# Optimization experiments

Measured on AMD Instinct MI355X. Metric: run time of the kernel, lower is better.

## Reference

```python
import jax, jax.numpy as jnp
import numpy as np

N = 1024
D = 128          # node_dim
NUM_LAYERS = 3
H_CLS = 128      # edge classifier hidden


def setup_inputs() -> dict:
    key = jax.random.key(0)
    ks = jax.random.split(key, 20)
    s_in = 1.0 / np.sqrt(3.0)
    s_d = 1.0 / np.sqrt(D)
    s_2d = 1.0 / np.sqrt(2 * D)
    s_h = 1.0 / np.sqrt(H_CLS)
    inp = {
        "node_features": jax.random.uniform(ks[0], (N, 3), jnp.float32),
        "adj_matrix": jax.random.uniform(ks[1], (N, N), jnp.float32),
        "edge_weights": jax.random.normal(ks[2], (N, N, 1), jnp.float32),
        # node embedding Linear(3, D)
        "W_embed": jax.random.uniform(ks[3], (3, D), jnp.float32, -s_in, s_in),
        "b_embed": jax.random.uniform(ks[4], (D,), jnp.float32, -s_in, s_in),
        # stacked GCN layer params, [L, ...]
        "Wu": jax.random.uniform(ks[5], (NUM_LAYERS, D, D), jnp.float32, -s_d, s_d),
        "bu": jax.random.uniform(ks[6], (NUM_LAYERS, D), jnp.float32, -s_d, s_d),
        "Wv": jax.random.uniform(ks[7], (NUM_LAYERS, D, D), jnp.float32, -s_d, s_d),
        "bv": jax.random.uniform(ks[8], (NUM_LAYERS, D), jnp.float32, -s_d, s_d),
        "Wg": jax.random.uniform(ks[9], (NUM_LAYERS, 2 * D, D), jnp.float32, -s_2d, s_2d),
        "bg": jax.random.uniform(ks[10], (NUM_LAYERS, D), jnp.float32, -s_2d, s_2d),
        # edge classifier: Linear(2D, 128) -> ReLU -> Linear(128, 1)
        "Wc1": jax.random.uniform(ks[11], (2 * D, H_CLS), jnp.float32, -s_2d, s_2d),
        "bc1": jax.random.uniform(ks[12], (H_CLS,), jnp.float32, -s_2d, s_2d),
        "Wc2": jax.random.uniform(ks[13], (H_CLS, 1), jnp.float32, -s_h, s_h),
        "bc2": jax.random.uniform(ks[14], (1,), jnp.float32, -s_h, s_h),
    }
    return inp


def reference(node_features, adj_matrix, edge_weights,
              W_embed, b_embed, Wu, bu, Wv, bv, Wg, bg,
              Wc1, bc1, Wc2, bc2):
    h = node_features @ W_embed + b_embed                       # [N, D]
    for l in range(NUM_LAYERS):
        u = h @ Wu[l] + bu[l]                                   # [N, D]
        v = h @ Wv[l] + bv[l]                                   # [N, D]
        agg = adj_matrix @ v                                    # [N, D]
        # gate Linear(2D, D) on cat([u, agg]) == u @ Wg[:D] + agg @ Wg[D:]
        gate = jax.nn.sigmoid(u @ Wg[l, :D] + agg @ Wg[l, D:] + bg[l])
        h = jax.nn.relu(h + gate * agg)
    # edge classifier: cat([h_i, h_j]) @ Wc1 == (h @ Wc1[:D])[i] + (h @ Wc1[D:])[j]
    hi = h @ Wc1[:D]                                            # [N, H]
    hj = h @ Wc1[D:]                                            # [N, H]
    hidden = jax.nn.relu(hi[:, None, :] + hj[None, :, :] + bc1) # [N, N, H]
    logits = jnp.einsum('ijh,h->ij', hidden, Wc2[:, 0]) + bc2[0]  # [N, N]
    loss = jnp.mean(jnp.square(logits * adj_matrix - edge_weights[..., 0]))
    return logits, loss
```

## Files before the change

kernel.cpp:

```cpp
#include <hip/hip_runtime.h>

#define NN 1024
#define DD 128

typedef __attribute__((ext_vector_type(8))) __bf16 bf16x8;
typedef __attribute__((ext_vector_type(4))) float f32x4;

__device__ __forceinline__ float us2f(unsigned short b) { return __uint_as_float(((unsigned)b) << 16); }
__device__ __forceinline__ unsigned short f2bf(float f) {
    unsigned x = __float_as_uint(f);
    unsigned r = (x + 0x7fffu + ((x >> 16) & 1u)) >> 16;
    return (unsigned short)r;
}

__global__ __launch_bounds__(256) void k_prep(
    const float* __restrict__ adj, unsigned short* __restrict__ aH, unsigned short* __restrict__ aL)
{
    int idx = (blockIdx.x * 256 + threadIdx.x) * 4;
    float4 a = *(const float4*)(adj + idx);
    ushort4 hv, lv;
    hv.x = f2bf(a.x); lv.x = f2bf(a.x - us2f(hv.x));
    hv.y = f2bf(a.y); lv.y = f2bf(a.y - us2f(hv.y));
    hv.z = f2bf(a.z); lv.z = f2bf(a.z - us2f(hv.z));
    hv.w = f2bf(a.w); lv.w = f2bf(a.w - us2f(hv.w));
    *(ushort4*)(aH + idx) = hv;
    *(ushort4*)(aL + idx) = lv;
}

__global__ __launch_bounds__(256) void k_embed(
    const float* __restrict__ nf, const float* __restrict__ We,
    const float* __restrict__ be, float* __restrict__ h)
{
    int tid = threadIdx.x;
    int m = blockIdx.x * 2 + (tid >> 7);
    int d = tid & 127;
    float a = be[d];
#pragma unroll
    for (int k = 0; k < 3; ++k) a = fmaf(nf[m * 3 + k], We[k * DD + d], a);
    h[m * DD + d] = a;
}

__global__ __launch_bounds__(256) void k_uv(
    const float* __restrict__ h,
    const float* __restrict__ Wu, const float* __restrict__ bu,
    const float* __restrict__ Wv, const float* __restrict__ bv,
    float* __restrict__ u, unsigned short* __restrict__ vTh, unsigned short* __restrict__ vTl)
{
    int tid = threadIdx.x;
    int d = tid & 127, half = tid >> 7;
    int m0 = blockIdx.x * 4;
    const float* W = half ? Wv : Wu;
    const float* A = h + m0 * DD;
    float acc[4] = {0.f, 0.f, 0.f, 0.f};
#pragma unroll 8
    for (int k = 0; k < DD; ++k) {
        float w = W[k * DD + d];
#pragma unroll
        for (int r = 0; r < 4; ++r) acc[r] = fmaf(A[r * DD + k], w, acc[r]);
    }
    if (half == 0) {
        float bb = bu[d];
#pragma unroll
        for (int r = 0; r < 4; ++r) u[(m0 + r) * DD + d] = acc[r] + bb;
    } else {
        float bb = bv[d];
        ushort4 hv, lv;
        float v0 = acc[0] + bb, v1 = acc[1] + bb, v2 = acc[2] + bb, v3 = acc[3] + bb;
        hv.x = f2bf(v0); lv.x = f2bf(v0 - us2f(hv.x));
        hv.y = f2bf(v1); lv.y = f2bf(v1 - us2f(hv.y));
        hv.z = f2bf(v2); lv.z = f2bf(v2 - us2f(hv.z));
        hv.w = f2bf(v3); lv.w = f2bf(v3 - us2f(hv.w));
        *(ushort4*)(vTh + d * NN + m0) = hv;
        *(ushort4*)(vTl + d * NN + m0) = lv;
    }
}

__global__ __launch_bounds__(64) void k_agg(
    const unsigned short* __restrict__ adjH, const unsigned short* __restrict__ adjL,
    const unsigned short* __restrict__ vTh, const unsigned short* __restrict__ vTl,
    float* __restrict__ agg)
{
    int lane = threadIdx.x;
    int b = blockIdx.x;
    int nt = (b >> 3) & 7;
    int mt = (b & 7) | ((b >> 6) << 3);
    int m = lane & 15, quad = lane >> 4;
    const unsigned short* ah = adjH + (size_t)(mt * 16 + m) * NN + quad * 8;
    const unsigned short* al = adjL + (size_t)(mt * 16 + m) * NN + quad * 8;
    const unsigned short* bh = vTh + (size_t)(nt * 16 + m) * NN + quad * 8;
    const unsigned short* bl = vTl + (size_t)(nt * 16 + m) * NN + quad * 8;
    f32x4 acc = {0.f, 0.f, 0.f, 0.f};
#pragma unroll 4
    for (int kt = 0; kt < 32; ++kt) {
        bf16x8 aH = *(const bf16x8*)(ah + kt * 32);
        bf16x8 aL = *(const bf16x8*)(al + kt * 32);
        bf16x8 bH = *(const bf16x8*)(bh + kt * 32);
        bf16x8 bL = *(const bf16x8*)(bl + kt * 32);
        acc = __builtin_amdgcn_mfma_f32_16x16x32_bf16(aH, bH, acc, 0, 0, 0);
        acc = __builtin_amdgcn_mfma_f32_16x16x32_bf16(aH, bL, acc, 0, 0, 0);
        acc = __builtin_amdgcn_mfma_f32_16x16x32_bf16(aL, bH, acc, 0, 0, 0);
    }
    int row0 = mt * 16 + quad * 4;
    int col = nt * 16 + m;
#pragma unroll
    for (int r = 0; r < 4; ++r) agg[(row0 + r) * DD + col] = acc[r];
}

__global__ __launch_bounds__(256) void k_gate(
    const float* __restrict__ u, const float* __restrict__ agg,
    const float* __restrict__ Wg, const float* __restrict__ bg,
    float* __restrict__ h)
{
    int tid = threadIdx.x;
    int d = tid & 127, rh = tid >> 7;
    int m0 = blockIdx.x * 4 + rh * 2;
    const float* WA = Wg;
    const float* WB = Wg + DD * DD;
    const float* Au = u + m0 * DD;
    const float* Ag = agg + m0 * DD;
    float acc[2] = {0.f, 0.f};
#pragma unroll 8
    for (int k = 0; k < DD; ++k) {
        float wa = WA[k * DD + d];
        float wb = WB[k * DD + d];
#pragma unroll
        for (int r = 0; r < 2; ++r)
            acc[r] = fmaf(Au[r * DD + k], wa, fmaf(Ag[r * DD + k], wb, acc[r]));
    }
    float bgd = bg[d];
#pragma unroll
    for (int r = 0; r < 2; ++r) {
        float z = acc[r] + bgd;
        float g = 1.f / (1.f + __expf(-z));
        float av = agg[(m0 + r) * DD + d];
        float hv = h[(m0 + r) * DD + d];
        float nh = fmaf(g, av, hv);
        h[(m0 + r) * DD + d] = nh > 0.f ? nh : 0.f;
    }
}

__global__ __launch_bounds__(256) void k_cls(
    const float* __restrict__ h,
    const float* __restrict__ Wc1, const float* __restrict__ bc1,
    const float* __restrict__ Wc2,
    float* __restrict__ hi, float* __restrict__ hj,
    float* __restrict__ S1, float* __restrict__ S2)
{
    __shared__ float sred[2][4];
    int tid = threadIdx.x;
    int hh = tid & 127, half = tid >> 7;
    int m0 = blockIdx.x * 4;
    if (tid < 8) sred[tid >> 2][tid & 3] = 0.f;
    __syncthreads();
    const float* W = Wc1 + (half ? DD * DD : 0);
    const float* A = h + m0 * DD;
    float acc[4] = {0.f, 0.f, 0.f, 0.f};
#pragma unroll 8
    for (int k = 0; k < DD; ++k) {
        float w = W[k * DD + hh];
#pragma unroll
        for (int r = 0; r < 4; ++r) acc[r] = fmaf(A[r * DD + k], w, acc[r]);
    }
    float wv = Wc2[hh];
    float bcv = half ? 0.f : bc1[hh];
    float* out = half ? hj : hi;
#pragma unroll
    for (int r = 0; r < 4; ++r) {
        float val = acc[r] + bcv;
        out[(m0 + r) * DD + hh] = val;
        float p = val * wv;
#pragma unroll
        for (int off = 32; off; off >>= 1) p += __shfl_down(p, off);
        if ((tid & 63) == 0) atomicAdd(&sred[half][r], p);
    }
    __syncthreads();
    if (tid < 4) S1[m0 + tid] = sred[0][tid];
    else if (tid < 8) S2[m0 + tid - 4] = sred[1][tid - 4];
}

__global__ __launch_bounds__(256) void k_edge(
    const float* __restrict__ hi, const float* __restrict__ hj,
    const float* __restrict__ S1, const float* __restrict__ S2,
    const float* __restrict__ Wc2, const float* __restrict__ bc2,
    const float* __restrict__ adj, const float* __restrict__ ew,
    float* __restrict__ outL, float* __restrict__ lossAcc)
{
    __shared__ float hiT[128][68];
    __shared__ float hjT[128][68];
    __shared__ float wS[128];
    __shared__ float lred;
    int tid = threadIdx.x;
    int i0 = (blockIdx.x >> 4) * 64, j0 = (blockIdx.x & 15) * 64;
    if (tid == 0) lred = 0.f;
    if (tid < 128) wS[tid] = Wc2[tid];
    for (int e = tid; e < 64 * 128; e += 256) {
        int r = e >> 7, hh = e & 127;
        hiT[hh][r] = hi[(i0 + r) * DD + hh];
        hjT[hh][r] = hj[(j0 + r) * DD + hh];
    }
    __syncthreads();
    int tx = tid & 15, ty = tid >> 4;
    float acc[4][4] = {};
#pragma unroll 4
    for (int hh = 0; hh < 128; ++hh) {
        f32x4 a = *(const f32x4*)&hiT[hh][ty * 4];
        f32x4 b = *(const f32x4*)&hjT[hh][tx * 4];
        float w = wS[hh];
#pragma unroll
        for (int p = 0; p < 4; ++p)
#pragma unroll
            for (int q = 0; q < 4; ++q) {
                float x = a[p] + b[q];
                acc[p][q] = fmaf(fabsf(x), w, acc[p][q]);
            }
    }
    float bcv = bc2[0];
    float ls = 0.f;
#pragma unroll
    for (int p = 0; p < 4; ++p) {
        int i = i0 + ty * 4 + p;
        float s1 = S1[i];
        int jb = j0 + tx * 4;
        f32x4 s2 = *(const f32x4*)(S2 + jb);
        f32x4 lg;
#pragma unroll
        for (int q = 0; q < 4; ++q)
            lg[q] = fmaf(0.5f, acc[p][q] + s1 + s2[q], bcv);
        *(f32x4*)(outL + (size_t)i * NN + jb) = lg;
        f32x4 a4 = *(const f32x4*)(adj + (size_t)i * NN + jb);
        f32x4 e4 = *(const f32x4*)(ew + (size_t)i * NN + jb);
#pragma unroll
        for (int q = 0; q < 4; ++q) {
            float t = fmaf(lg[q], a4[q], -e4[q]);
            ls = fmaf(t, t, ls);
        }
    }
#pragma unroll
    for (int off = 32; off; off >>= 1) ls += __shfl_down(ls, off);
    if ((tid & 63) == 0) atomicAdd(&lred, ls);
    __syncthreads();
    if (tid == 0) atomicAdd(lossAcc, lred);
}

__global__ void k_loss(const float* __restrict__ lossAcc, float* __restrict__ outL)
{
    if (threadIdx.x == 0 && blockIdx.x == 0)
        outL[(size_t)NN * NN] = lossAcc[0] * (1.f / (1024.f * 1024.f));
}

extern "C" void kernel_launch(void* const* d_in, const int* in_sizes, int n_in,
                              void* d_out, int out_size, void* d_ws, size_t ws_size,
                              hipStream_t stream)
{
    const float* nf  = (const float*)d_in[0];
    const float* adj = (const float*)d_in[1];
    const float* ew  = (const float*)d_in[2];
    const float* We  = (const float*)d_in[3];
    const float* be  = (const float*)d_in[4];
    const float* Wu  = (const float*)d_in[5];
    const float* bu  = (const float*)d_in[6];
    const float* Wv  = (const float*)d_in[7];
    const float* bv  = (const float*)d_in[8];
    const float* Wg  = (const float*)d_in[9];
    const float* bg  = (const float*)d_in[10];
    const float* Wc1 = (const float*)d_in[11];
    const float* bc1 = (const float*)d_in[12];
    const float* Wc2 = (const float*)d_in[13];
    const float* bc2 = (const float*)d_in[14];

    float* ws = (float*)d_ws;
    float* h   = ws;
    float* u   = ws + 131072;
    unsigned short* vTh = (unsigned short*)(ws + 262144);
    unsigned short* vTl = (unsigned short*)(ws + 327680);
    float* agg = ws + 393216;
    unsigned short* adjH = (unsigned short*)(ws + 524288);
    unsigned short* adjL = (unsigned short*)(ws + 1048576);
    float* S1  = ws + 1572864;
    float* S2  = ws + 1573888;
    float* lossAcc = ws + 1574912;
    float* hi = u;
    float* hj = agg;

    hipMemsetAsync(lossAcc, 0, sizeof(float), stream);
    k_prep<<<1024, 256, 0, stream>>>(adj, adjH, adjL);
    k_embed<<<512, 256, 0, stream>>>(nf, We, be, h);
    for (int l = 0; l < 3; ++l) {
        k_uv<<<256, 256, 0, stream>>>(h, Wu + l * 16384, bu + l * 128,
                                      Wv + l * 16384, bv + l * 128, u, vTh, vTl);
        k_agg<<<512, 64, 0, stream>>>(adjH, adjL, vTh, vTl, agg);
        k_gate<<<256, 256, 0, stream>>>(u, agg, Wg + l * 32768, bg + l * 128, h);
    }
    k_cls<<<256, 256, 0, stream>>>(h, Wc1, bc1, Wc2, hi, hj, S1, S2);
    k_edge<<<256, 256, 0, stream>>>(hi, hj, S1, S2, Wc2, bc2, adj, ew,
                                    (float*)d_out, lossAcc);
    k_loss<<<1, 64, 0, stream>>>(lossAcc, (float*)d_out);
}
```

Baseline: 208.2 us.

## Fuse per-layer kernels, split-K the aggregation, fold loss finalize into edge kernel

Merges the adjacency split, embedding and first u/v projection into one launch. The gate of layer l is fused with the u/v projection of layer l+1, and the last gate with the classifier projection. The adjacency aggregation becomes an 8-way split-K over 1024 blocks writing partial sums that the gate kernel reduces. The memset and the separate loss kernel are replaced by a last-block counter inside the edge kernel. This removes many launches and adds parallelism to the skinny aggregation GEMM, at the cost of extra partial-sum traffic (8x N×D floats) and a redundant per-block embedding recompute.

```diff
diff --git a/kernel.cpp b/kernel.cpp
--- a/kernel.cpp
+++ b/kernel.cpp
@@ -9,54 +9,64 @@
 __device__ __forceinline__ float us2f(unsigned short b) { return __uint_as_float(((unsigned)b) << 16); }
 __device__ __forceinline__ unsigned short f2bf(float f) {
     unsigned x = __float_as_uint(f);
-    unsigned r = (x + 0x7fffu + ((x >> 16) & 1u)) >> 16;
-    return (unsigned short)r;
-}
-
-__global__ __launch_bounds__(256) void k_prep(
-    const float* __restrict__ adj, unsigned short* __restrict__ aH, unsigned short* __restrict__ aL)
-{
-    int idx = (blockIdx.x * 256 + threadIdx.x) * 4;
-    float4 a = *(const float4*)(adj + idx);
-    ushort4 hv, lv;
-    hv.x = f2bf(a.x); lv.x = f2bf(a.x - us2f(hv.x));
-    hv.y = f2bf(a.y); lv.y = f2bf(a.y - us2f(hv.y));
-    hv.z = f2bf(a.z); lv.z = f2bf(a.z - us2f(hv.z));
-    hv.w = f2bf(a.w); lv.w = f2bf(a.w - us2f(hv.w));
-    *(ushort4*)(aH + idx) = hv;
-    *(ushort4*)(aL + idx) = lv;
-}
-
-__global__ __launch_bounds__(256) void k_embed(
-    const float* __restrict__ nf, const float* __restrict__ We,
-    const float* __restrict__ be, float* __restrict__ h)
-{
-    int tid = threadIdx.x;
-    int m = blockIdx.x * 2 + (tid >> 7);
-    int d = tid & 127;
-    float a = be[d];
-#pragma unroll
-    for (int k = 0; k < 3; ++k) a = fmaf(nf[m * 3 + k], We[k * DD + d], a);
-    h[m * DD + d] = a;
-}
-
-__global__ __launch_bounds__(256) void k_uv(
-    const float* __restrict__ h,
+    return (unsigned short)((x + 0x7fffu + ((x >> 16) & 1u)) >> 16);
+}
+
+__global__ __launch_bounds__(256) void k_prep_embuv(
+    const float* __restrict__ adj, unsigned short* __restrict__ aH, unsigned short* __restrict__ aL,
+    const float* __restrict__ nf, const float* __restrict__ We, const float* __restrict__ be,
     const float* __restrict__ Wu, const float* __restrict__ bu,
     const float* __restrict__ Wv, const float* __restrict__ bv,
-    float* __restrict__ u, unsigned short* __restrict__ vTh, unsigned short* __restrict__ vTl)
-{
-    int tid = threadIdx.x;
+    float* __restrict__ h, float* __restrict__ u,
+    unsigned short* __restrict__ vTh, unsigned short* __restrict__ vTl,
+    float* __restrict__ lossAcc, unsigned* __restrict__ counter)
+{
+    __shared__ float hS[4][DD];
+    int b = blockIdx.x, tid = threadIdx.x;
+    if (b < 1024) {
+        int idx = (b * 256 + tid) * 4;
+        float4 a = *(const float4*)(adj + idx);
+        ushort4 hv, lv;
+        hv.x = f2bf(a.x); lv.x = f2bf(a.x - us2f(hv.x));
+        hv.y = f2bf(a.y); lv.y = f2bf(a.y - us2f(hv.y));
+        hv.z = f2bf(a.z); lv.z = f2bf(a.z - us2f(hv.z));
+        hv.w = f2bf(a.w); lv.w = f2bf(a.w - us2f(hv.w));
+        *(ushort4*)(aH + idx) = hv;
+        *(ushort4*)(aL + idx) = lv;
+        if (b == 0 && tid == 0) { *lossAcc = 0.f; *counter = 0u; }
+        return;
+    }
+    int m0 = (b - 1024) * 4;
     int d = tid & 127, half = tid >> 7;
-    int m0 = blockIdx.x * 4;
+    float hr[4];
+#pragma unroll
+    for (int r = 0; r < 4; ++r) {
+        float a = be[d];
+#pragma unroll
+        for (int k = 0; k < 3; ++k) a = fmaf(nf[(m0 + r) * 3 + k], We[k * DD + d], a);
+        hr[r] = a;
+    }
+    if (half == 0) {
+#pragma unroll
+        for (int r = 0; r < 4; ++r) { h[(m0 + r) * DD + d] = hr[r]; hS[r][d] = hr[r]; }
+    }
+    __syncthreads();
     const float* W = half ? Wv : Wu;
-    const float* A = h + m0 * DD;
     float acc[4] = {0.f, 0.f, 0.f, 0.f};
-#pragma unroll 8
-    for (int k = 0; k < DD; ++k) {
-        float w = W[k * DD + d];
-#pragma unroll
-        for (int r = 0; r < 4; ++r) acc[r] = fmaf(A[r * DD + k], w, acc[r]);
+#pragma unroll 4
+    for (int k4 = 0; k4 < DD; k4 += 4) {
+        f32x4 h0 = *(const f32x4*)&hS[0][k4];
+        f32x4 h1 = *(const f32x4*)&hS[1][k4];
+        f32x4 h2 = *(const f32x4*)&hS[2][k4];
+        f32x4 h3 = *(const f32x4*)&hS[3][k4];
+#pragma unroll
+        for (int kk = 0; kk < 4; ++kk) {
+            float w = W[(k4 + kk) * DD + d];
+            acc[0] = fmaf(h0[kk], w, acc[0]);
+            acc[1] = fmaf(h1[kk], w, acc[1]);
+            acc[2] = fmaf(h2[kk], w, acc[2]);
+            acc[3] = fmaf(h3[kk], w, acc[3]);
+        }
     }
     if (half == 0) {
         float bb = bu[d];
@@ -64,8 +74,8 @@
         for (int r = 0; r < 4; ++r) u[(m0 + r) * DD + d] = acc[r] + bb;
     } else {
         float bb = bv[d];
+        float v0 = acc[0] + bb, v1 = acc[1] + bb, v2 = acc[2] + bb, v3 = acc[3] + bb;
         ushort4 hv, lv;
-        float v0 = acc[0] + bb, v1 = acc[1] + bb, v2 = acc[2] + bb, v3 = acc[3] + bb;
         hv.x = f2bf(v0); lv.x = f2bf(v0 - us2f(hv.x));
         hv.y = f2bf(v1); lv.y = f2bf(v1 - us2f(hv.y));
         hv.z = f2bf(v2); lv.z = f2bf(v2 - us2f(hv.z));
@@ -75,23 +85,25 @@
     }
 }
 
-__global__ __launch_bounds__(64) void k_agg(
+__global__ __launch_bounds__(256) void k_agg(
     const unsigned short* __restrict__ adjH, const unsigned short* __restrict__ adjL,
     const unsigned short* __restrict__ vTh, const unsigned short* __restrict__ vTl,
-    float* __restrict__ agg)
-{
-    int lane = threadIdx.x;
+    float* __restrict__ P)
+{
+    int tid = threadIdx.x, lane = tid & 63, w = tid >> 6;
     int b = blockIdx.x;
-    int nt = (b >> 3) & 7;
-    int mt = (b & 7) | ((b >> 6) << 3);
+    int nt = b >> 7;
+    int mt = (b >> 1) & 63;
+    int kc = ((b & 1) << 2) | w;
     int m = lane & 15, quad = lane >> 4;
-    const unsigned short* ah = adjH + (size_t)(mt * 16 + m) * NN + quad * 8;
-    const unsigned short* al = adjL + (size_t)(mt * 16 + m) * NN + quad * 8;
-    const unsigned short* bh = vTh + (size_t)(nt * 16 + m) * NN + quad * 8;
-    const unsigned short* bl = vTl + (size_t)(nt * 16 + m) * NN + quad * 8;
+    int k0 = kc * 128 + quad * 8;
+    const unsigned short* ah = adjH + (size_t)(mt * 16 + m) * NN + k0;
+    const unsigned short* al = adjL + (size_t)(mt * 16 + m) * NN + k0;
+    const unsigned short* bh = vTh + (size_t)(nt * 16 + m) * NN + k0;
+    const unsigned short* bl = vTl + (size_t)(nt * 16 + m) * NN + k0;
     f32x4 acc = {0.f, 0.f, 0.f, 0.f};
-#pragma unroll 4
-    for (int kt = 0; kt < 32; ++kt) {
+#pragma unroll
+    for (int kt = 0; kt < 4; ++kt) {
         bf16x8 aH = *(const bf16x8*)(ah + kt * 32);
         bf16x8 aL = *(const bf16x8*)(al + kt * 32);
         bf16x8 bH = *(const bf16x8*)(bh + kt * 32);
@@ -100,78 +112,179 @@
         acc = __builtin_amdgcn_mfma_f32_16x16x32_bf16(aH, bL, acc, 0, 0, 0);
         acc = __builtin_amdgcn_mfma_f32_16x16x32_bf16(aL, bH, acc, 0, 0, 0);
     }
+    float* Pk = P + (size_t)kc * (NN * DD);
     int row0 = mt * 16 + quad * 4;
     int col = nt * 16 + m;
 #pragma unroll
-    for (int r = 0; r < 4; ++r) agg[(row0 + r) * DD + col] = acc[r];
-}
-
-__global__ __launch_bounds__(256) void k_gate(
-    const float* __restrict__ u, const float* __restrict__ agg,
+    for (int r = 0; r < 4; ++r) Pk[(row0 + r) * DD + col] = acc[r];
+}
+
+__global__ __launch_bounds__(256) void k_gateuv(
+    const float* __restrict__ P, float* __restrict__ u, float* __restrict__ h,
     const float* __restrict__ Wg, const float* __restrict__ bg,
-    float* __restrict__ h)
-{
+    const float* __restrict__ Wun, const float* __restrict__ bun,
+    const float* __restrict__ Wvn, const float* __restrict__ bvn,
+    unsigned short* __restrict__ vTh, unsigned short* __restrict__ vTl)
+{
+    __shared__ float uS[4][DD], aS[4][DD], hS[4][DD];
     int tid = threadIdx.x;
-    int d = tid & 127, rh = tid >> 7;
-    int m0 = blockIdx.x * 4 + rh * 2;
+    int m0 = blockIdx.x * 4;
+    int d = tid & 127, half = tid >> 7;
+#pragma unroll
+    for (int e = tid; e < 512; e += 256) {
+        int r = e >> 7, dd = e & 127;
+        int idx = (m0 + r) * DD + dd;
+        float s = 0.f;
+#pragma unroll
+        for (int c = 0; c < 8; ++c) s += P[(size_t)c * (NN * DD) + idx];
+        aS[r][dd] = s;
+        uS[r][dd] = u[idx];
+    }
+    __syncthreads();
     const float* WA = Wg;
     const float* WB = Wg + DD * DD;
-    const float* Au = u + m0 * DD;
-    const float* Ag = agg + m0 * DD;
+    int r0 = half * 2;
     float acc[2] = {0.f, 0.f};
-#pragma unroll 8
-    for (int k = 0; k < DD; ++k) {
-        float wa = WA[k * DD + d];
-        float wb = WB[k * DD + d];
-#pragma unroll
-        for (int r = 0; r < 2; ++r)
-            acc[r] = fmaf(Au[r * DD + k], wa, fmaf(Ag[r * DD + k], wb, acc[r]));
+#pragma unroll 4
+    for (int k4 = 0; k4 < DD; k4 += 4) {
+        f32x4 u0 = *(const f32x4*)&uS[r0][k4];
+        f32x4 u1 = *(const f32x4*)&uS[r0 + 1][k4];
+        f32x4 a0 = *(const f32x4*)&aS[r0][k4];
+        f32x4 a1 = *(const f32x4*)&aS[r0 + 1][k4];
+#pragma unroll
+        for (int kk = 0; kk < 4; ++kk) {
+            float wa = WA[(k4 + kk) * DD + d];
+            float wb = WB[(k4 + kk) * DD + d];
+            acc[0] = fmaf(u0[kk], wa, fmaf(a0[kk], wb, acc[0]));
+            acc[1] = fmaf(u1[kk], wa, fmaf(a1[kk], wb, acc[1]));
+        }
     }
     float bgd = bg[d];
 #pragma unroll
-    for (int r = 0; r < 2; ++r) {
-        float z = acc[r] + bgd;
-        float g = 1.f / (1.f + __expf(-z));
-        float av = agg[(m0 + r) * DD + d];
-        float hv = h[(m0 + r) * DD + d];
-        float nh = fmaf(g, av, hv);
-        h[(m0 + r) * DD + d] = nh > 0.f ? nh : 0.f;
-    }
-}
-
-__global__ __launch_bounds__(256) void k_cls(
-    const float* __restrict__ h,
-    const float* __restrict__ Wc1, const float* __restrict__ bc1,
-    const float* __restrict__ Wc2,
+    for (int rr = 0; rr < 2; ++rr) {
+        int r = r0 + rr;
+        float g = 1.f / (1.f + __expf(-(acc[rr] + bgd)));
+        float nh = fmaf(g, aS[r][d], h[(m0 + r) * DD + d]);
+        nh = nh > 0.f ? nh : 0.f;
+        h[(m0 + r) * DD + d] = nh;
+        hS[r][d] = nh;
+    }
+    __syncthreads();
+    const float* W = half ? Wvn : Wun;
+    float av[4] = {0.f, 0.f, 0.f, 0.f};
+#pragma unroll 4
+    for (int k4 = 0; k4 < DD; k4 += 4) {
+        f32x4 h0 = *(const f32x4*)&hS[0][k4];
+        f32x4 h1 = *(const f32x4*)&hS[1][k4];
+        f32x4 h2 = *(const f32x4*)&hS[2][k4];
+        f32x4 h3 = *(const f32x4*)&hS[3][k4];
+#pragma unroll
+        for (int kk = 0; kk < 4; ++kk) {
+            float w = W[(k4 + kk) * DD + d];
+            av[0] = fmaf(h0[kk], w, av[0]);
+            av[1] = fmaf(h1[kk], w, av[1]);
+            av[2] = fmaf(h2[kk], w, av[2]);
+            av[3] = fmaf(h3[kk], w, av[3]);
+        }
+    }
+    if (half == 0) {
+        float bb = bun[d];
+#pragma unroll
+        for (int r = 0; r < 4; ++r) u[(m0 + r) * DD + d] = av[r] + bb;
+    } else {
+        float bb = bvn[d];
+        float v0 = av[0] + bb, v1 = av[1] + bb, v2 = av[2] + bb, v3 = av[3] + bb;
+        ushort4 hv, lv;
+        hv.x = f2bf(v0); lv.x = f2bf(v0 - us2f(hv.x));
+        hv.y = f2bf(v1); lv.y = f2bf(v1 - us2f(hv.y));
+        hv.z = f2bf(v2); lv.z = f2bf(v2 - us2f(hv.z));
+        hv.w = f2bf(v3); lv.w = f2bf(v3 - us2f(hv.w));
+        *(ushort4*)(vTh + d * NN + m0) = hv;
+        *(ushort4*)(vTl + d * NN + m0) = lv;
+    }
+}
+
+__global__ __launch_bounds__(256) void k_gatecls(
+    const float* __restrict__ P, float* __restrict__ u, float* __restrict__ h,
+    const float* __restrict__ Wg, const float* __restrict__ bg,
+    const float* __restrict__ Wc1, const float* __restrict__ bc1, const float* __restrict__ Wc2,
     float* __restrict__ hi, float* __restrict__ hj,
     float* __restrict__ S1, float* __restrict__ S2)
 {
+    __shared__ float uS[4][DD], aS[4][DD], hS[4][DD];
     __shared__ float sred[2][4];
     int tid = threadIdx.x;
-    int hh = tid & 127, half = tid >> 7;
     int m0 = blockIdx.x * 4;
+    int d = tid & 127, half = tid >> 7;
     if (tid < 8) sred[tid >> 2][tid & 3] = 0.f;
+#pragma unroll
+    for (int e = tid; e < 512; e += 256) {
+        int r = e >> 7, dd = e & 127;
+        int idx = (m0 + r) * DD + dd;
+        float s = 0.f;
+#pragma unroll
+        for (int c = 0; c < 8; ++c) s += P[(size_t)c * (NN * DD) + idx];
+        aS[r][dd] = s;
+        uS[r][dd] = u[idx];
+    }
+    __syncthreads();
+    const float* WA = Wg;
+    const float* WB = Wg + DD * DD;
+    int r0 = half * 2;
+    float acc[2] = {0.f, 0.f};
+#pragma unroll 4
+    for (int k4 = 0; k4 < DD; k4 += 4) {
+        f32x4 u0 = *(const f32x4*)&uS[r0][k4];
+        f32x4 u1 = *(const f32x4*)&uS[r0 + 1][k4];
+        f32x4 a0 = *(const f32x4*)&aS[r0][k4];
+        f32x4 a1 = *(const f32x4*)&aS[r0 + 1][k4];
+#pragma unroll
+        for (int kk = 0; kk < 4; ++kk) {
+            float wa = WA[(k4 + kk) * DD + d];
+            float wb = WB[(k4 + kk) * DD + d];
+            acc[0] = fmaf(u0[kk], wa, fmaf(a0[kk], wb, acc[0]));
+            acc[1] = fmaf(u1[kk], wa, fmaf(a1[kk], wb, acc[1]));
+        }
+    }
+    float bgd = bg[d];
+#pragma unroll
+    for (int rr = 0; rr < 2; ++rr) {
+        int r = r0 + rr;
+        float g = 1.f / (1.f + __expf(-(acc[rr] + bgd)));
+        float nh = fmaf(g, aS[r][d], h[(m0 + r) * DD + d]);
+        nh = nh > 0.f ? nh : 0.f;
+        hS[r][d] = nh;
+    }
     __syncthreads();
     const float* W = Wc1 + (half ? DD * DD : 0);
-    const float* A = h + m0 * DD;
-    float acc[4] = {0.f, 0.f, 0.f, 0.f};
-#pragma unroll 8
-    for (int k = 0; k < DD; ++k) {
-        float w = W[k * DD + hh];
-#pragma unroll
-        for (int r = 0; r < 4; ++r) acc[r] = fmaf(A[r * DD + k], w, acc[r]);
-    }
-    float wv = Wc2[hh];
-    float bcv = half ? 0.f : bc1[hh];
+    float av[4] = {0.f, 0.f, 0.f, 0.f};
+#pragma unroll 4
+    for (int k4 = 0; k4 < DD; k4 += 4) {
+        f32x4 h0 = *(const f32x4*)&hS[0][k4];
+        f32x4 h1 = *(const f32x4*)&hS[1][k4];
+        f32x4 h2 = *(const f32x4*)&hS[2][k4];
+        f32x4 h3 = *(const f32x4*)&hS[3][k4];
+#pragma unroll
+        for (int kk = 0; kk < 4; ++kk) {
+            float w = W[(k4 + kk) * DD + d];
+            av[0] = fmaf(h0[kk], w, av[0]);
+            av[1] = fmaf(h1[kk], w, av[1]);
+            av[2] = fmaf(h2[kk], w, av[2]);
+            av[3] = fmaf(h3[kk], w, av[3]);
+        }
+    }
+    float wv = Wc2[d];
+    float bcv = half ? 0.f : bc1[d];
     float* out = half ? hj : hi;
+    int lane = tid & 63;
 #pragma unroll
     for (int r = 0; r < 4; ++r) {
-        float val = acc[r] + bcv;
-        out[(m0 + r) * DD + hh] = val;
+        float val = av[r] + bcv;
+        out[(m0 + r) * DD + d] = val;
         float p = val * wv;
 #pragma unroll
         for (int off = 32; off; off >>= 1) p += __shfl_down(p, off);
-        if ((tid & 63) == 0) atomicAdd(&sred[half][r], p);
+        if (lane == 0) atomicAdd(&sred[half][r], p);
     }
     __syncthreads();
     if (tid < 4) S1[m0 + tid] = sred[0][tid];
@@ -183,7 +296,7 @@
     const float* __restrict__ S1, const float* __restrict__ S2,
     const float* __restrict__ Wc2, const float* __restrict__ bc2,
     const float* __restrict__ adj, const float* __restrict__ ew,
-    float* __restrict__ outL, float* __restrict__ lossAcc)
+    float* __restrict__ outL, float* __restrict__ lossAcc, unsigned* __restrict__ counter)
 {
     __shared__ float hiT[128][68];
     __shared__ float hjT[128][68];
@@ -239,13 +352,15 @@
     for (int off = 32; off; off >>= 1) ls += __shfl_down(ls, off);
     if ((tid & 63) == 0) atomicAdd(&lred, ls);
     __syncthreads();
-    if (tid == 0) atomicAdd(lossAcc, lred);
-}
-
-__global__ void k_loss(const float* __restrict__ lossAcc, float* __restrict__ outL)
-{
-    if (threadIdx.x == 0 && blockIdx.x == 0)
-        outL[(size_t)NN * NN] = lossAcc[0] * (1.f / (1024.f * 1024.f));
+    if (tid == 0) {
+        atomicAdd(lossAcc, lred);
+        __threadfence();
+        unsigned old = atomicAdd(counter, 1u);
+        if (old == 255u) {
+            __threadfence();
+            outL[(size_t)NN * NN] = (*(volatile float*)lossAcc) * (1.f / (1024.f * 1024.f));
+        }
+    }
 }
 
 extern "C" void kernel_launch(void* const* d_in, const int* in_sizes, int n_in,
@@ -273,26 +388,29 @@
     float* u   = ws + 131072;
     unsigned short* vTh = (unsigned short*)(ws + 262144);
     unsigned short* vTl = (unsigned short*)(ws + 327680);
-    float* agg = ws + 393216;
-    unsigned short* adjH = (unsigned short*)(ws + 524288);
-    unsigned short* adjL = (unsigned short*)(ws + 1048576);
-    float* S1  = ws + 1572864;
-    float* S2  = ws + 1573888;
-    float* lossAcc = ws + 1574912;
-    float* hi = u;
-    float* hj = agg;
-
-    hipMemsetAsync(lossAcc, 0, sizeof(float), stream);
-    k_prep<<<1024, 256, 0, stream>>>(adj, adjH, adjL);
-    k_embed<<<512, 256, 0, stream>>>(nf, We, be, h);
+    float* P   = ws + 393216;
+    unsigned short* adjH = (unsigned short*)(ws + 1441792);
+    unsigned short* adjL = (unsigned short*)(ws + 1966080);
+    float* hi  = ws + 2490368;
+    float* hj  = ws + 2621440;
+    float* S1  = ws + 2752512;
+    float* S2  = ws + 2753536;
+    float* lossAcc = ws + 2754560;
+    unsigned* counter = (unsigned*)(ws + 2754561);
+
+    k_prep_embuv<<<1280, 256, 0, stream>>>(adj, adjH, adjL, nf, We, be,
+                                           Wu, bu, Wv, bv, h, u, vTh, vTl, lossAcc, counter);
     for (int l = 0; l < 3; ++l) {
-        k_uv<<<256, 256, 0, stream>>>(h, Wu + l * 16384, bu + l * 128,
-                                      Wv + l * 16384, bv + l * 128, u, vTh, vTl);
-        k_agg<<<512, 64, 0, stream>>>(adjH, adjL, vTh, vTl, agg);
-        k_gate<<<256, 256, 0, stream>>>(u, agg, Wg + l * 32768, bg + l * 128, h);
-    }
-    k_cls<<<256, 256, 0, stream>>>(h, Wc1, bc1, Wc2, hi, hj, S1, S2);
+        k_agg<<<1024, 256, 0, stream>>>(adjH, adjL, vTh, vTl, P);
+        if (l < 2)
+            k_gateuv<<<256, 256, 0, stream>>>(P, u, h, Wg + l * 32768, bg + l * 128,
+                                              Wu + (l + 1) * 16384, bu + (l + 1) * 128,
+                                              Wv + (l + 1) * 16384, bv + (l + 1) * 128,
+                                              vTh, vTl);
+        else
+            k_gatecls<<<256, 256, 0, stream>>>(P, u, h, Wg + 2 * 32768, bg + 2 * 128,
+                                               Wc1, bc1, Wc2, hi, hj, S1, S2);
+    }
     k_edge<<<256, 256, 0, stream>>>(hi, hj, S1, S2, Wc2, bc2, adj, ew,
-                                    (float*)d_out, lossAcc);
-    k_loss<<<1, 64, 0, stream>>>(lossAcc, (float*)d_out);
-}
+                                    (float*)d_out, lossAcc, counter);
+}
```

New measurement: 187.2 us. -10.1%, faster.
